# Optimization experiments

Measured on AMD Instinct MI355X. Metric: run time of the kernel, lower is better.

The kernel has to match this reference:

```python
import jax, jax.numpy as jnp
import numpy as np

L = 12; D = 768; H = 12; HD = 64; FF = 3072; P = 16; IMG = 224; BLK = 64
LORA = 16.0 / 64.0  # lora_alpha / r
PD = 512; B = 8


def _ln(x, g, b, eps=1e-6):
    m = x.mean(-1, keepdims=True)
    v = ((x - m) ** 2).mean(-1, keepdims=True)
    return (x - m) * jax.lax.rsqrt(v + eps) * g + b


def _dq(q, s):
    # int4 codes [O, I] + blockwise absmax-style scales [O, I//BLK] -> fp32 weight
    O, I = q.shape
    return ((q.astype(jnp.float32).reshape(O, I // BLK, BLK) - 7.5) * s[:, :, None]).reshape(O, I)


def _forward(img, patch_w, patch_b, cls_token, ln1_g, ln1_b, ln2_g, ln2_b, g1, g2,
             qkv_s, qkv_b, a_qkv, b_qkv, proj_s, proj_b, a_proj, b_proj,
             fc1_s, fc1_b, fc2_s, fc2_b, fcn_g, fcn_b, head_w, head_b,
             qkv_q, proj_q, fc1_q, fc2_q):
    x = img[:, 0]                                   # [B,3,224,224]
    Bn = x.shape[0]
    gp = IMG // P
    # patch embed (conv16x16/s16 == unfold + matmul)
    p = x.reshape(Bn, 3, gp, P, gp, P).transpose(0, 2, 4, 1, 3, 5).reshape(Bn, gp * gp, 3 * P * P)
    tok = p @ patch_w.T + patch_b                   # [B,196,768]
    cls = jnp.broadcast_to(cls_token, (Bn, 1, D))
    x = jnp.concatenate([cls, tok], axis=1)         # [B,197,768]

    def block(x, pr):
        (l1g, l1b, l2g, l2b, gm1, gm2, qq, qs, qb, aQ, bQ,
         pq, ps, pb, aP, bP, f1q, f1s, f1b, f2q, f2s, f2b) = pr
        h = _ln(x, l1g, l1b)
        # fused dequant + matmul + LoRA (qkv)
        qkv = h @ _dq(qq, qs).T + qb + LORA * ((h @ aQ.T) @ bQ.T)  # [B,N,3D]
        q, k, v = jnp.split(qkv, 3, axis=-1)
        heads = lambda t: t.reshape(Bn, -1, H, HD).transpose(0, 2, 1, 3)
        q, k, v = heads(q), heads(k), heads(v)
        attn = jax.nn.softmax(jnp.einsum('bhnd,bhmd->bhnm', q, k) / np.sqrt(HD).astype(np.float32), axis=-1)
        o = jnp.einsum('bhnm,bhmd->bhnd', attn, v).transpose(0, 2, 1, 3).reshape(Bn, -1, D)
        # dequant + matmul + LoRA (attn out proj)
        o = o @ _dq(pq, ps).T + pb + LORA * ((o @ aP.T) @ bP.T)
        x = x + gm1 * o                             # layerscale residual
        h = _ln(x, l2g, l2b)
        h = jax.nn.gelu(h @ _dq(f1q, f1s).T + f1b)
        h = h @ _dq(f2q, f2s).T + f2b
        x = x + gm2 * h
        return x, None

    xs = (ln1_g, ln1_b, ln2_g, ln2_b, g1, g2, qkv_q, qkv_s, qkv_b, a_qkv, b_qkv,
          proj_q, proj_s, proj_b, a_proj, b_proj, fc1_q, fc1_s, fc1_b, fc2_q, fc2_s, fc2_b)
    x, _ = jax.lax.scan(block, x, xs)
    pooled = x[:, 1:].mean(axis=1)                  # BEiT avg-pool over patch tokens
    pooled = _ln(pooled, fcn_g, fcn_b)              # fc_norm
    return jax.nn.relu(pooled @ head_w.T + head_b)  # Linear + ReLU projection -> [B,512]


def setup_inputs() -> dict:
    key = jax.random.key(0)
    ks = jax.random.split(key, 24)
    f = lambda i, sh, sc=0.02: jax.random.normal(ks[i], sh, dtype=jnp.float32) * sc
    u = lambda i, sh: jax.random.uniform(ks[i], sh, dtype=jnp.float32) * 0.01 + 1e-3
    qi = lambda i, sh: jax.random.randint(ks[i], sh, 0, 16, dtype=jnp.int32)
    return {
        'img': f(0, (B, 1, 3, IMG, IMG), 1.0),
        'patch_w': f(1, (D, 3 * P * P)), 'patch_b': jnp.zeros((D,), jnp.float32),
        'cls_token': f(2, (1, 1, D)),
        'ln1_g': jnp.ones((L, D), jnp.float32), 'ln1_b': jnp.zeros((L, D), jnp.float32),
        'ln2_g': jnp.ones((L, D), jnp.float32), 'ln2_b': jnp.zeros((L, D), jnp.float32),
        'g1': jnp.full((L, D), 0.1, jnp.float32), 'g2': jnp.full((L, D), 0.1, jnp.float32),
        'qkv_q': qi(3, (L, 3 * D, D)), 'qkv_s': u(4, (L, 3 * D, D // BLK)), 'qkv_b': f(5, (L, 3 * D)),
        'a_qkv': f(6, (L, 64, D)), 'b_qkv': f(7, (L, 3 * D, 64)),
        'proj_q': qi(8, (L, D, D)), 'proj_s': u(9, (L, D, D // BLK)), 'proj_b': jnp.zeros((L, D), jnp.float32),
        'a_proj': f(10, (L, 64, D)), 'b_proj': f(11, (L, D, 64)),
        'fc1_q': qi(12, (L, FF, D)), 'fc1_s': u(13, (L, FF, D // BLK)), 'fc1_b': jnp.zeros((L, FF), jnp.float32),
        'fc2_q': qi(14, (L, D, FF)), 'fc2_s': u(15, (L, D, FF // BLK)), 'fc2_b': jnp.zeros((L, D), jnp.float32),
        'fcn_g': jnp.ones((D,), jnp.float32), 'fcn_b': jnp.zeros((D,), jnp.float32),
        'head_w': f(16, (PD, D)), 'head_b': jnp.zeros((PD,), jnp.float32),
    }


def reference(img, patch_w, patch_b, cls_token, ln1_g, ln1_b, ln2_g, ln2_b, g1, g2,
              qkv_q, qkv_s, qkv_b, a_qkv, b_qkv, proj_q, proj_s, proj_b, a_proj, b_proj,
              fc1_q, fc1_s, fc1_b, fc2_q, fc2_s, fc2_b, fcn_g, fcn_b, head_w, head_b):
    return _forward(img, patch_w, patch_b, cls_token, ln1_g, ln1_b, ln2_g, ln2_b, g1, g2,
                    qkv_s, qkv_b, a_qkv, b_qkv, proj_s, proj_b, a_proj, b_proj,
                    fc1_s, fc1_b, fc2_s, fc2_b, fcn_g, fcn_b, head_w, head_b,
                    qkv_q, proj_q, fc1_q, fc2_q)
```

## Files before the change

### kernel.cpp

```cpp
#include <hip/hip_runtime.h>
#include <hip/hip_bf16.h>

using bf16 = __hip_bfloat16;
typedef __attribute__((ext_vector_type(8))) short short8;
typedef __attribute__((ext_vector_type(4))) float f32x4;

#define NTOK 197
#define MTOK 1576
#define MPATCH 1568
#define UROWS 102400

static __device__ __forceinline__ float bf2f(bf16 v){ return __bfloat162float(v); }
static __device__ __forceinline__ bf16 f2bf(float v){ return __float2bfloat16(v); }
static __device__ __forceinline__ unsigned pk2(float a, float b){
  union{ bf16 h[2]; unsigned u; } r; r.h[0]=f2bf(a); r.h[1]=f2bf(b); return r.u;
}

static __device__ __forceinline__ float gelu_tanh(float x){
  float x3 = x*x*x;
  float a = 0.7978845608028654f*(x + 0.044715f*x3);
  float e = __expf(-2.f*fabsf(a));
  float t = (1.f-e)/(1.f+e);
  t = (a >= 0.f) ? t : -t;
  return 0.5f*x*(1.f+t);
}

static __device__ __forceinline__ void gload16(const void* g, void* l){
  __builtin_amdgcn_global_load_lds(
      (const __attribute__((address_space(1))) unsigned*)g,
      (__attribute__((address_space(3))) unsigned*)l, 16, 0, 0);
}

template<int N> static __device__ __forceinline__ void wait_vm(){
  if constexpr (N==3)      asm volatile("s_waitcnt vmcnt(3)" ::: "memory");
  else if constexpr (N==5) asm volatile("s_waitcnt vmcnt(5)" ::: "memory");
  else                     asm volatile("s_waitcnt vmcnt(0)" ::: "memory");
}

__global__ void dq_k(const int* __restrict__ q, const float* __restrict__ s,
                     bf16* __restrict__ o, int rows, int K){
  long total8 = (long)rows * K / 8;
  for (long i = blockIdx.x*256 + threadIdx.x; i < total8; i += (long)gridDim.x*256){
    long e0 = i*8;
    int n = (int)(e0 / K), k = (int)(e0 % K);
    int4 a = *(const int4*)(q + (size_t)n*K + k);
    int4 b = *(const int4*)(q + (size_t)n*K + k + 4);
    float sc = s[(size_t)n*(K>>6) + (k>>6)];
    uint4 r;
    r.x = pk2(((float)a.x-7.5f)*sc, ((float)a.y-7.5f)*sc);
    r.y = pk2(((float)a.z-7.5f)*sc, ((float)a.w-7.5f)*sc);
    r.z = pk2(((float)b.x-7.5f)*sc, ((float)b.y-7.5f)*sc);
    r.w = pk2(((float)b.z-7.5f)*sc, ((float)b.w-7.5f)*sc);
    *(uint4*)(o + (size_t)n*K + k) = r;
  }
}

__global__ void cvt_k(const float* __restrict__ in, bf16* __restrict__ out, int n4){
  for (int i = blockIdx.x*256 + threadIdx.x; i < n4; i += gridDim.x*256){
    float4 v = *(const float4*)(in + (size_t)i*4);
    uint2 r; r.x = pk2(v.x, v.y); r.y = pk2(v.z, v.w);
    *(uint2*)(out + (size_t)i*4) = r;
  }
}

__global__ void usum_k(const float* __restrict__ part, bf16* __restrict__ ub){
  int i = blockIdx.x*256 + threadIdx.x;
  if (i >= MTOK*64/4) return;
  float4 s = {0.f,0.f,0.f,0.f};
  #pragma unroll
  for (int pz=0;pz<4;pz++){
    float4 v = *(const float4*)(part + (size_t)pz*UROWS + (size_t)i*4);
    s.x+=v.x; s.y+=v.y; s.z+=v.z; s.w+=v.w;
  }
  uint2 r; r.x = pk2(0.25f*s.x, 0.25f*s.y); r.y = pk2(0.25f*s.z, 0.25f*s.w);
  *(uint2*)(ub + (size_t)i*4) = r;
}

__global__ void patchify_k(const float* __restrict__ img, bf16* __restrict__ p){
  int idx = blockIdx.x*256 + threadIdx.x;
  if (idx >= MPATCH*768) return;
  int col = idx % 768, pr = idx / 768;
  int b = pr / 196, patch = pr % 196;
  int c = col >> 8, rem = col & 255, py = rem >> 4, px = rem & 15;
  int gy = patch / 14, gx = patch % 14;
  float v = img[(((size_t)(b*3 + c))*224 + gy*16 + py)*224 + gx*16 + px];
  p[idx] = f2bf(v);
}

__global__ void assemble_k(const float* __restrict__ tok, const float* __restrict__ cls,
                           float* __restrict__ x){
  int idx = blockIdx.x*256 + threadIdx.x;
  if (idx >= MTOK*768) return;
  int d = idx % 768, row = idx / 768;
  int b = row / NTOK, r = row % NTOK;
  x[idx] = (r == 0) ? cls[d] : tok[((size_t)(b*196) + r - 1)*768 + d];
}

__global__ __launch_bounds__(256) void ln_k(const float* __restrict__ x,
                                            const float* __restrict__ g,
                                            const float* __restrict__ b,
                                            bf16* __restrict__ out, int M){
  int row = blockIdx.x*4 + (threadIdx.x >> 6);
  int lane = threadIdx.x & 63;
  if (row >= M) return;
  const float* xr = x + (size_t)row*768;
  float4 v[3]; float s = 0.f;
  #pragma unroll
  for (int j=0;j<3;j++){
    v[j] = *(const float4*)(xr + lane*4 + j*256);
    s += v[j].x + v[j].y + v[j].z + v[j].w;
  }
  #pragma unroll
  for (int o=32;o;o>>=1) s += __shfl_xor(s, o);
  float mean = s * (1.f/768.f);
  float vs = 0.f;
  #pragma unroll
  for (int j=0;j<3;j++){
    float dx=v[j].x-mean, dy=v[j].y-mean, dz=v[j].z-mean, dw=v[j].w-mean;
    vs += dx*dx + dy*dy + dz*dz + dw*dw;
  }
  #pragma unroll
  for (int o=32;o;o>>=1) vs += __shfl_xor(vs, o);
  float rs = rsqrtf(vs*(1.f/768.f) + 1e-6f);
  bf16* orow = out + (size_t)row*768;
  #pragma unroll
  for (int j=0;j<3;j++){
    int d0 = lane*4 + j*256;
    float4 gv = *(const float4*)(g + d0);
    float4 bv = *(const float4*)(b + d0);
    uint2 pk;
    pk.x = pk2((v[j].x-mean)*rs*gv.x + bv.x, (v[j].y-mean)*rs*gv.y + bv.y);
    pk.y = pk2((v[j].z-mean)*rs*gv.z + bv.z, (v[j].w-mean)*rs*gv.w + bv.w);
    *(uint2*)(orow + d0) = pk;
  }
}

__global__ __launch_bounds__(256) void attn_k(const bf16* __restrict__ qkv, bf16* __restrict__ o){
  __shared__ char Kc[2][32*128];
  __shared__ bf16 Vt[2][64][40];
  __shared__ bf16 Pl[4][32][40];

  const int blk = blockIdx.x;
  const int half = blk & 1, bh = blk >> 1;
  const int b = bh / 12, h = bh % 12;
  const int t = threadIdx.x, wave = t>>6, lane = t&63;
  const int qbase = half*128 + wave*32;
  const bf16* base = qkv + (size_t)b*NTOK*2304 + h*64;

  short8 qf[2][2];
  #pragma unroll
  for (int qt=0;qt<2;qt++){
    int row = qbase + qt*16 + (lane&15); row = row < NTOK ? row : NTOK-1;
    const bf16* qr = base + (size_t)row*2304 + (lane>>4)*8;
    qf[qt][0] = *(const short8*)(qr);
    qf[qt][1] = *(const short8*)(qr + 32);
  }

  f32x4 Oa[2][4];
  float mrow[2][4], srow[2][4];
  #pragma unroll
  for (int i=0;i<2;i++)
    #pragma unroll
    for (int j=0;j<4;j++){ Oa[i][j] = (f32x4){0.f,0.f,0.f,0.f}; }
  #pragma unroll
  for (int i=0;i<2;i++)
    #pragma unroll
    for (int j=0;j<4;j++){ mrow[i][j] = -1e30f; srow[i][j] = 0.f; }

  const int sr = t>>3, sc = (t&7)*8;
  auto ldK = [&](int c)->uint4{
    int kv = c*32 + sr; kv = kv < NTOK ? kv : NTOK-1;
    return *(const uint4*)(base + (size_t)kv*2304 + 768 + sc);
  };
  auto ldV = [&](int c)->uint4{
    int kv = c*32 + sr;
    uint4 r = {0,0,0,0};
    if (kv < NTOK) r = *(const uint4*)(base + (size_t)kv*2304 + 1536 + sc);
    return r;
  };
  auto wrK = [&](int buf, uint4 kvv){
    *(uint4*)(Kc[buf] + sr*128 + ((sc*2) ^ ((sr&7)<<4))) = kvv;
  };
  auto wrV = [&](int buf, uint4 vvv){
    union{ uint4 u; short s[8]; } w; w.u = vvv;
    #pragma unroll
    for (int j=0;j<8;j++) *(short*)&Vt[buf][sc+j][sr] = w.s[j];
  };

  { uint4 k0 = ldK(0), v0 = ldV(0); wrK(0,k0); wrV(0,v0); }
  __syncthreads();

  for (int c=0;c<7;c++){
    const int buf = c & 1;
    uint4 kn, vn; const bool pf = (c < 6);
    if (pf){ kn = ldK(c+1); vn = ldV(c+1); }

    f32x4 S[2][2];
    #pragma unroll
    for (int i=0;i<2;i++)
      #pragma unroll
      for (int j=0;j<2;j++) S[i][j] = (f32x4){0.f,0.f,0.f,0.f};
    #pragma unroll
    for (int kt=0;kt<2;kt++){
      int rk = kt*16 + (lane&15);
      const char* kb = Kc[buf] + rk*128;
      int swz = (rk&7)<<4;
      short8 b0 = *(const short8*)(kb + (((lane>>4)*16) ^ swz));
      short8 b1 = *(const short8*)(kb + ((64 + (lane>>4)*16) ^ swz));
      #pragma unroll
      for (int qt=0;qt<2;qt++){
        S[qt][kt] = __builtin_amdgcn_mfma_f32_16x16x32_bf16(qf[qt][0], b0, S[qt][kt],0,0,0);
        S[qt][kt] = __builtin_amdgcn_mfma_f32_16x16x32_bf16(qf[qt][1], b1, S[qt][kt],0,0,0);
      }
    }

    #pragma unroll
    for (int qt=0;qt<2;qt++){
      #pragma unroll
      for (int r=0;r<4;r++){
        float s0 = S[qt][0][r]*0.125f, s1 = S[qt][1][r]*0.125f;
        if (c == 6){
          if (192 + (lane&15) >= NTOK) s0 = -1e30f;
          s1 = -1e30f;
        }
        float mx = fmaxf(s0, s1);
        mx = fmaxf(mx, __shfl_xor(mx,1));
        mx = fmaxf(mx, __shfl_xor(mx,2));
        mx = fmaxf(mx, __shfl_xor(mx,4));
        mx = fmaxf(mx, __shfl_xor(mx,8));
        float mo = mrow[qt][r];
        float mn = fmaxf(mo, mx);
        float scl = __expf(mo - mn);
        mrow[qt][r] = mn;
        float p0 = __expf(s0 - mn), p1 = __expf(s1 - mn);
        srow[qt][r] = srow[qt][r]*scl + p0 + p1;
        #pragma unroll
        for (int dt=0;dt<4;dt++) Oa[qt][dt][r] *= scl;
        int pr = qt*16 + (lane>>4)*4 + r;
        Pl[wave][pr][lane&15]      = f2bf(p0);
        Pl[wave][pr][16+(lane&15)] = f2bf(p1);
      }
    }

    short8 vb[4];
    #pragma unroll
    for (int dt=0;dt<4;dt++)
      vb[dt] = *(const short8*)(&Vt[buf][dt*16+(lane&15)][(lane>>4)*8]);
    #pragma unroll
    for (int qt=0;qt<2;qt++){
      short8 pa = *(const short8*)(&Pl[wave][qt*16+(lane&15)][(lane>>4)*8]);
      #pragma unroll
      for (int dt=0;dt<4;dt++)
        Oa[qt][dt] = __builtin_amdgcn_mfma_f32_16x16x32_bf16(pa, vb[dt], Oa[qt][dt],0,0,0);
    }

    if (pf){ wrK(buf^1, kn); wrV(buf^1, vn); }
    __syncthreads();
  }

  #pragma unroll
  for (int qt=0;qt<2;qt++)
    #pragma unroll
    for (int r=0;r<4;r++){
      float s = srow[qt][r];
      s += __shfl_xor(s,1); s += __shfl_xor(s,2);
      s += __shfl_xor(s,4); s += __shfl_xor(s,8);
      srow[qt][r] = 1.f/s;
    }
  #pragma unroll
  for (int qt=0;qt<2;qt++){
    #pragma unroll
    for (int r=0;r<4;r++){
      int tok = qbase + qt*16 + (lane>>4)*4 + r;
      if (tok < NTOK){
        bf16* orow = o + ((size_t)(b*NTOK+tok))*768 + h*64 + (lane&15);
        float inv = srow[qt][r];
        #pragma unroll
        for (int dt=0;dt<4;dt++) orow[dt*16] = f2bf(Oa[qt][dt][r]*inv);
      }
    }
  }
}

__global__ void pool_k(const float* __restrict__ x, float* __restrict__ pooled){
  int idx = blockIdx.x*256 + threadIdx.x;
  if (idx >= 8*768) return;
  int b = idx / 768, d = idx % 768;
  float s = 0.f;
  for (int i=1;i<NTOK;i++) s += x[((size_t)(b*NTOK)+i)*768 + d];
  pooled[idx] = s * (1.f/196.f);
}

template<int BM, int BN, int LORA, int OUTMODE, int ACT>
__global__ __launch_bounds__(256) void gemm_k(
    const bf16* __restrict__ A, const bf16* __restrict__ W,
    const bf16* __restrict__ ulora, const bf16* __restrict__ Blora,
    const float* __restrict__ bias, const float* __restrict__ gvec,
    void* __restrict__ Cout,
    int M, int N, int Kst, int kiters, size_t kslab)
{
  constexpr int WCM = BM/2;
  constexpr int WCN = BN/2;
  constexpr int FM  = WCM/16;
  constexpr int FN  = WCN/16;
  constexpr int NW  = BN/32;
  constexpr int LCNT = 1 + NW;

  __shared__ char As[2][BM*128];
  __shared__ char Bs[2][BN*128];

  int mt, nt;
  {
    int gmy = gridDim.y;
    int nwg = gridDim.x * gmy;
    int bid = blockIdx.y * gridDim.x + blockIdx.x;
    int q8 = nwg >> 3, r8 = nwg & 7, xcd = bid & 7, idx = bid >> 3;
    int swz = (xcd < r8 ? xcd*(q8+1) : r8*(q8+1) + (xcd-r8)*q8) + idx;
    nt = swz / gmy; mt = swz - nt*gmy;
  }
  const int kz = blockIdx.z;
  const int k0 = kz * kiters;
  const int t = threadIdx.x, wave = t>>6, lane = t&63;
  const int wr = wave>>1, wc = wave&1;
  const int KT = kiters + (LORA ? 1 : 0);

  const int srow = t >> 3;
  const int swzc = ((t&7)<<4) ^ ((srow&7)<<4);

  f32x4 acc[FM][FN];
  #pragma unroll
  for (int i=0;i<FM;i++)
    #pragma unroll
    for (int j=0;j<FN;j++) acc[i][j] = (f32x4){0.f,0.f,0.f,0.f};

  auto STAGE = [&](int it, int buf){
    {
      int gm = mt*BM + srow; gm = gm < M ? gm : M-1;
      const char* src = (LORA && it == kiters)
        ? (const char*)ulora + (size_t)gm*128 + swzc
        : (const char*)A + (size_t)gm*Kst*2 + (size_t)(k0+it)*128 + swzc;
      gload16(src, As[buf] + wave*1024);
    }
    #pragma unroll
    for (int c=0;c<NW;c++){
      int gn = nt*BN + 32*c + srow;
      const char* src = (LORA && it == kiters)
        ? (const char*)Blora + (size_t)gn*128 + swzc
        : (const char*)W + (size_t)gn*Kst*2 + (size_t)(k0+it)*128 + swzc;
      gload16(src, Bs[buf] + c*4096 + wave*1024);
    }
  };

  const int lrow = lane & 15;
  const int lkb  = (lane >> 4) * 16;
  auto computeTile = [&](int buf){
    __builtin_amdgcn_s_setprio(1);
    #pragma unroll
    for (int kk=0; kk<2; kk++){
      short8 af[FM]; short8 bw[FN];
      #pragma unroll
      for (int f=0; f<FM; f++){
        int ra = wr*WCM + f*16 + lrow;
        af[f] = *(const short8*)(As[buf] + ra*128 + ((kk*64 + lkb) ^ ((ra&7)<<4)));
      }
      #pragma unroll
      for (int f=0; f<FN; f++){
        int rb = wc*WCN + f*16 + lrow;
        bw[f] = *(const short8*)(Bs[buf] + rb*128 + ((kk*64 + lkb) ^ ((rb&7)<<4)));
      }
      #pragma unroll
      for (int i=0;i<FM;i++)
        #pragma unroll
        for (int j=0;j<FN;j++)
          acc[i][j] = __builtin_amdgcn_mfma_f32_16x16x32_bf16(af[i], bw[j], acc[i][j], 0, 0, 0);
    }
    __builtin_amdgcn_s_setprio(0);
  };

  STAGE(0, 0);
  if (KT > 1) STAGE(1, 1);

  for (int it = 0; it < KT; ++it){
    if (it == KT-1) wait_vm<0>(); else wait_vm<LCNT>();
    __builtin_amdgcn_s_barrier();
    computeTile(it & 1);
    asm volatile("s_waitcnt lgkmcnt(0)" ::: "memory");
    __builtin_amdgcn_s_barrier();
    if (it+2 < KT) STAGE(it+2, it & 1);
  }

  const int erow = (lane >> 4) * 4, ecol = lane & 15;
  #pragma unroll
  for (int i=0;i<FM;i++){
    #pragma unroll
    for (int j=0;j<FN;j++){
      int n = nt*BN + wc*WCN + j*16 + ecol;
      float bv = (bias != nullptr) ? bias[n] : 0.f;
      float gv = (OUTMODE==2) ? gvec[n] : 0.f;
      #pragma unroll
      for (int q=0; q<4; q++){
        int m = mt*BM + wr*WCM + i*16 + erow + q;
        if (m < M){
          float v = acc[i][j][q] + bv;
          if (ACT == 1) v = gelu_tanh(v);
          if (ACT == 2) v = fmaxf(v, 0.f);
          size_t off = (size_t)m*N + n;
          if (OUTMODE == 0)      ((float*)Cout)[(size_t)kz*kslab + off] = v;
          else if (OUTMODE == 1) ((bf16*)Cout)[off] = f2bf(v);
          else                   ((float*)Cout)[off] += gv * v;
        }
      }
    }
  }
}

extern "C" void kernel_launch(void* const* d_in, const int* in_sizes, int n_in,
                              void* d_out, int out_size, void* d_ws, size_t ws_size,
                              hipStream_t stream){
  (void)in_sizes; (void)n_in; (void)out_size; (void)ws_size;
  const float* img    = (const float*)d_in[0];
  const float* patchw = (const float*)d_in[1];
  const float* patchb = (const float*)d_in[2];
  const float* cls    = (const float*)d_in[3];
  const float* ln1g   = (const float*)d_in[4];
  const float* ln1b   = (const float*)d_in[5];
  const float* ln2g   = (const float*)d_in[6];
  const float* ln2b   = (const float*)d_in[7];
  const float* g1     = (const float*)d_in[8];
  const float* g2     = (const float*)d_in[9];
  const int*   qkvq   = (const int*)d_in[10];
  const float* qkvs   = (const float*)d_in[11];
  const float* qkvb   = (const float*)d_in[12];
  const float* aQ     = (const float*)d_in[13];
  const float* bQ     = (const float*)d_in[14];
  const int*   projq  = (const int*)d_in[15];
  const float* projs  = (const float*)d_in[16];
  const float* projb  = (const float*)d_in[17];
  const float* aP     = (const float*)d_in[18];
  const float* bP     = (const float*)d_in[19];
  const int*   fc1q   = (const int*)d_in[20];
  const float* fc1s   = (const float*)d_in[21];
  const float* fc1b   = (const float*)d_in[22];
  const int*   fc2q   = (const int*)d_in[23];
  const float* fc2s   = (const float*)d_in[24];
  const float* fc2b   = (const float*)d_in[25];
  const float* fcn_g  = (const float*)d_in[26];
  const float* fcn_b  = (const float*)d_in[27];
  const float* headw  = (const float*)d_in[28];
  const float* headb  = (const float*)d_in[29];
  float* out = (float*)d_out;

  char* wp = (char*)d_ws;
  auto alloc = [&](size_t bytes)->char* {
    char* r = wp; wp += (bytes + 255) & ~(size_t)255; return r;
  };
  float* x      = (float*)alloc((size_t)MTOK*768*4);
  bf16*  qkvo   = (bf16*) alloc((size_t)MTOK*2304*2);
  bf16*  h      = (bf16*) alloc((size_t)MTOK*768*2);
  bf16*  h1     = (bf16*) alloc((size_t)MTOK*3072*2);
  bf16*  ob     = (bf16*) alloc((size_t)MTOK*768*2);
  float* u_part = (float*)alloc((size_t)4*UROWS*4);
  bf16*  ub     = (bf16*) alloc((size_t)MTOK*64*2);
  bf16*  p      = (bf16*) alloc((size_t)MPATCH*768*2);
  float* tmp    = (float*)alloc((size_t)MTOK*768*4);
  float* pooled = (float*)alloc((size_t)8*768*4);
  bf16*  pooledb= (bf16*) alloc((size_t)8*768*2);
  bf16* wqb = (bf16*)alloc((size_t)12*2304*768*2);
  bf16* wpb = (bf16*)alloc((size_t)12*768*768*2);
  bf16* w1b = (bf16*)alloc((size_t)12*3072*768*2);
  bf16* w2b = (bf16*)alloc((size_t)12*768*3072*2);
  bf16* patchwb = (bf16*)alloc((size_t)768*768*2);
  bf16* headwb  = (bf16*)alloc((size_t)512*768*2);
  bf16* aQb = (bf16*)alloc((size_t)12*64*768*2);
  bf16* bQb = (bf16*)alloc((size_t)12*2304*64*2);
  bf16* aPb = (bf16*)alloc((size_t)12*64*768*2);
  bf16* bPb = (bf16*)alloc((size_t)12*768*64*2);

  const int GM32 = (MTOK + 31) / 32;

  dq_k<<<2048, 256, 0, stream>>>(qkvq, qkvs, wqb, 12*2304, 768);
  dq_k<<<2048, 256, 0, stream>>>(projq, projs, wpb, 12*768, 768);
  dq_k<<<2048, 256, 0, stream>>>(fc1q, fc1s, w1b, 12*3072, 768);
  dq_k<<<2048, 256, 0, stream>>>(fc2q, fc2s, w2b, 12*768, 3072);
  cvt_k<<<576, 256, 0, stream>>>(patchw, patchwb, 768*768/4);
  cvt_k<<<384, 256, 0, stream>>>(headw, headwb, 512*768/4);
  cvt_k<<<576, 256, 0, stream>>>(aQ, aQb, 12*64*768/4);
  cvt_k<<<1728, 256, 0, stream>>>(bQ, bQb, 12*2304*64/4);
  cvt_k<<<576, 256, 0, stream>>>(aP, aPb, 12*64*768/4);
  cvt_k<<<576, 256, 0, stream>>>(bP, bPb, 12*768*64/4);

  patchify_k<<<(MPATCH*768 + 255)/256, 256, 0, stream>>>(img, p);
  gemm_k<32,64,0,0,0><<<dim3(768/64, MPATCH/32, 1), 256, 0, stream>>>(
      p, patchwb, nullptr, nullptr, patchb, nullptr, tmp,
      MPATCH, 768, 768, 12, 0);
  assemble_k<<<(MTOK*768 + 255)/256, 256, 0, stream>>>(tmp, cls, x);

  for (int l=0; l<12; l++){
    const bf16* wq_l = wqb + (size_t)l*2304*768;
    const bf16* wp_l = wpb + (size_t)l*768*768;
    const bf16* w1_l = w1b + (size_t)l*3072*768;
    const bf16* w2_l = w2b + (size_t)l*768*3072;

    ln_k<<<(MTOK+3)/4, 256, 0, stream>>>(x, ln1g + l*768, ln1b + l*768, h, MTOK);
    gemm_k<32,64,0,0,0><<<dim3(1, GM32, 4), 256, 0, stream>>>(
        h, aQb + (size_t)l*64*768, nullptr, nullptr, nullptr, nullptr, u_part,
        MTOK, 64, 768, 3, UROWS);
    usum_k<<<(MTOK*64/4 + 255)/256, 256, 0, stream>>>(u_part, ub);
    gemm_k<32,128,1,1,0><<<dim3(2304/128, GM32, 1), 256, 0, stream>>>(
        h, wq_l, ub, bQb + (size_t)l*2304*64, qkvb + (size_t)l*2304,
        nullptr, qkvo, MTOK, 2304, 768, 12, 0);
    attn_k<<<192, 256, 0, stream>>>(qkvo, ob);
    gemm_k<32,64,0,0,0><<<dim3(1, GM32, 4), 256, 0, stream>>>(
        ob, aPb + (size_t)l*64*768, nullptr, nullptr, nullptr, nullptr, u_part,
        MTOK, 64, 768, 3, UROWS);
    usum_k<<<(MTOK*64/4 + 255)/256, 256, 0, stream>>>(u_part, ub);
    gemm_k<32,64,1,2,0><<<dim3(768/64, GM32, 1), 256, 0, stream>>>(
        ob, wp_l, ub, bPb + (size_t)l*768*64, projb + (size_t)l*768,
        g1 + l*768, x, MTOK, 768, 768, 12, 0);

    ln_k<<<(MTOK+3)/4, 256, 0, stream>>>(x, ln2g + l*768, ln2b + l*768, h, MTOK);
    gemm_k<32,128,0,1,1><<<dim3(3072/128, GM32, 1), 256, 0, stream>>>(
        h, w1_l, nullptr, nullptr, fc1b + (size_t)l*3072,
        nullptr, h1, MTOK, 3072, 768, 12, 0);
    gemm_k<32,64,0,2,0><<<dim3(768/64, GM32, 1), 256, 0, stream>>>(
        h1, w2_l, nullptr, nullptr, fc2b + (size_t)l*768,
        g2 + l*768, x, MTOK, 768, 3072, 48, 0);
  }

  pool_k<<<(8*768 + 255)/256, 256, 0, stream>>>(x, pooled);
  ln_k<<<2, 256, 0, stream>>>(pooled, fcn_g, fcn_b, pooledb, 8);
  gemm_k<32,128,0,0,2><<<dim3(512/128, 1, 1), 256, 0, stream>>>(
      pooledb, headwb, nullptr, nullptr, headb, nullptr, out,
      8, 512, 768, 12, 0);
}
```

Baseline: 1.739 ms.

## Fold LoRA adapters into dequantized qkv and proj weights once at setup

Computes W + 0.25*B@A for the qkv and output-projection weights with a per-layer batched GEMM during setup, and adds the result into the bf16 dequantized weights. The per-layer LoRA down-projection GEMMs, partial-sum reductions and the extra LoRA k-step in the main GEMMs are removed. The cost is one extra setup GEMM over all layers and an additional bf16 rounding of the merged weight, which may shift numerics slightly.

```diff
diff --git a/kernel.cpp b/kernel.cpp
--- a/kernel.cpp
+++ b/kernel.cpp
@@ -8,7 +8,6 @@
 #define NTOK 197
 #define MTOK 1576
 #define MPATCH 1568
-#define UROWS 102400
 
 static __device__ __forceinline__ float bf2f(bf16 v){ return __bfloat162float(v); }
 static __device__ __forceinline__ bf16 f2bf(float v){ return __float2bfloat16(v); }
@@ -55,25 +54,23 @@
   }
 }
 
-__global__ void cvt_k(const float* __restrict__ in, bf16* __restrict__ out, int n4){
+__global__ void cvt_k(const float* __restrict__ in, bf16* __restrict__ out, int n4, float a){
   for (int i = blockIdx.x*256 + threadIdx.x; i < n4; i += gridDim.x*256){
     float4 v = *(const float4*)(in + (size_t)i*4);
-    uint2 r; r.x = pk2(v.x, v.y); r.y = pk2(v.z, v.w);
+    uint2 r; r.x = pk2(v.x*a, v.y*a); r.y = pk2(v.z*a, v.w*a);
     *(uint2*)(out + (size_t)i*4) = r;
   }
 }
 
-__global__ void usum_k(const float* __restrict__ part, bf16* __restrict__ ub){
-  int i = blockIdx.x*256 + threadIdx.x;
-  if (i >= MTOK*64/4) return;
-  float4 s = {0.f,0.f,0.f,0.f};
-  #pragma unroll
-  for (int pz=0;pz<4;pz++){
-    float4 v = *(const float4*)(part + (size_t)pz*UROWS + (size_t)i*4);
-    s.x+=v.x; s.y+=v.y; s.z+=v.z; s.w+=v.w;
-  }
-  uint2 r; r.x = pk2(0.25f*s.x, 0.25f*s.y); r.y = pk2(0.25f*s.z, 0.25f*s.w);
-  *(uint2*)(ub + (size_t)i*4) = r;
+__global__ void trans_k(const float* __restrict__ in, bf16* __restrict__ out,
+                        int L, int R, int C){
+  long total = (long)L*R*C;
+  for (long i = blockIdx.x*256 + threadIdx.x; i < total; i += (long)gridDim.x*256){
+    long rc = (long)R*C;
+    int l = (int)(i / rc); long rem = i % rc;
+    int c = (int)(rem / R), r = (int)(rem % R);
+    out[i] = f2bf(in[(size_t)l*rc + (size_t)r*C + c]);
+  }
 }
 
 __global__ void patchify_k(const float* __restrict__ img, bf16* __restrict__ p){
@@ -291,10 +288,9 @@
   pooled[idx] = s * (1.f/196.f);
 }
 
-template<int BM, int BN, int LORA, int OUTMODE, int ACT>
+template<int BM, int BN, int OUTMODE, int ACT, int FOLD>
 __global__ __launch_bounds__(256) void gemm_k(
     const bf16* __restrict__ A, const bf16* __restrict__ W,
-    const bf16* __restrict__ ulora, const bf16* __restrict__ Blora,
     const float* __restrict__ bias, const float* __restrict__ gvec,
     void* __restrict__ Cout,
     int M, int N, int Kst, int kiters, size_t kslab)
@@ -318,11 +314,15 @@
     int swz = (xcd < r8 ? xcd*(q8+1) : r8*(q8+1) + (xcd-r8)*q8) + idx;
     nt = swz / gmy; mt = swz - nt*gmy;
   }
-  const int kz = blockIdx.z;
+  if (FOLD){
+    A += (size_t)blockIdx.z * (size_t)M * 64;
+    W += (size_t)blockIdx.z * (size_t)N * 64;
+  }
+  const int kz = FOLD ? 0 : blockIdx.z;
   const int k0 = kz * kiters;
   const int t = threadIdx.x, wave = t>>6, lane = t&63;
   const int wr = wave>>1, wc = wave&1;
-  const int KT = kiters + (LORA ? 1 : 0);
+  const int KT = kiters;
 
   const int srow = t >> 3;
   const int swzc = ((t&7)<<4) ^ ((srow&7)<<4);
@@ -336,18 +336,14 @@
   auto STAGE = [&](int it, int buf){
     {
       int gm = mt*BM + srow; gm = gm < M ? gm : M-1;
-      const char* src = (LORA && it == kiters)
-        ? (const char*)ulora + (size_t)gm*128 + swzc
-        : (const char*)A + (size_t)gm*Kst*2 + (size_t)(k0+it)*128 + swzc;
-      gload16(src, As[buf] + wave*1024);
+      gload16((const char*)A + (size_t)gm*Kst*2 + (size_t)(k0+it)*128 + swzc,
+              As[buf] + wave*1024);
     }
     #pragma unroll
     for (int c=0;c<NW;c++){
       int gn = nt*BN + 32*c + srow;
-      const char* src = (LORA && it == kiters)
-        ? (const char*)Blora + (size_t)gn*128 + swzc
-        : (const char*)W + (size_t)gn*Kst*2 + (size_t)(k0+it)*128 + swzc;
-      gload16(src, Bs[buf] + c*4096 + wave*1024);
+      gload16((const char*)W + (size_t)gn*Kst*2 + (size_t)(k0+it)*128 + swzc,
+              Bs[buf] + c*4096 + wave*1024);
     }
   };
 
@@ -407,7 +403,11 @@
           size_t off = (size_t)m*N + n;
           if (OUTMODE == 0)      ((float*)Cout)[(size_t)kz*kslab + off] = v;
           else if (OUTMODE == 1) ((bf16*)Cout)[off] = f2bf(v);
-          else                   ((float*)Cout)[off] += gv * v;
+          else if (OUTMODE == 2) ((float*)Cout)[off] += gv * v;
+          else {
+            bf16* C = (bf16*)Cout + (FOLD ? (size_t)blockIdx.z*(size_t)M*N : (size_t)0);
+            C[off] = f2bf(bf2f(C[off]) + v);
+          }
         }
       }
     }
@@ -459,8 +459,6 @@
   bf16*  h      = (bf16*) alloc((size_t)MTOK*768*2);
   bf16*  h1     = (bf16*) alloc((size_t)MTOK*3072*2);
   bf16*  ob     = (bf16*) alloc((size_t)MTOK*768*2);
-  float* u_part = (float*)alloc((size_t)4*UROWS*4);
-  bf16*  ub     = (bf16*) alloc((size_t)MTOK*64*2);
   bf16*  p      = (bf16*) alloc((size_t)MPATCH*768*2);
   float* tmp    = (float*)alloc((size_t)MTOK*768*4);
   float* pooled = (float*)alloc((size_t)8*768*4);
@@ -471,10 +469,10 @@
   bf16* w2b = (bf16*)alloc((size_t)12*768*3072*2);
   bf16* patchwb = (bf16*)alloc((size_t)768*768*2);
   bf16* headwb  = (bf16*)alloc((size_t)512*768*2);
-  bf16* aQb = (bf16*)alloc((size_t)12*64*768*2);
-  bf16* bQb = (bf16*)alloc((size_t)12*2304*64*2);
-  bf16* aPb = (bf16*)alloc((size_t)12*64*768*2);
-  bf16* bPb = (bf16*)alloc((size_t)12*768*64*2);
+  bf16* bQs = (bf16*)alloc((size_t)12*2304*64*2);
+  bf16* bPs = (bf16*)alloc((size_t)12*768*64*2);
+  bf16* aQT = (bf16*)alloc((size_t)12*768*64*2);
+  bf16* aPT = (bf16*)alloc((size_t)12*768*64*2);
 
   const int GM32 = (MTOK + 31) / 32;
 
@@ -482,17 +480,20 @@
   dq_k<<<2048, 256, 0, stream>>>(projq, projs, wpb, 12*768, 768);
   dq_k<<<2048, 256, 0, stream>>>(fc1q, fc1s, w1b, 12*3072, 768);
   dq_k<<<2048, 256, 0, stream>>>(fc2q, fc2s, w2b, 12*768, 3072);
-  cvt_k<<<576, 256, 0, stream>>>(patchw, patchwb, 768*768/4);
-  cvt_k<<<384, 256, 0, stream>>>(headw, headwb, 512*768/4);
-  cvt_k<<<576, 256, 0, stream>>>(aQ, aQb, 12*64*768/4);
-  cvt_k<<<1728, 256, 0, stream>>>(bQ, bQb, 12*2304*64/4);
-  cvt_k<<<576, 256, 0, stream>>>(aP, aPb, 12*64*768/4);
-  cvt_k<<<576, 256, 0, stream>>>(bP, bPb, 12*768*64/4);
+  cvt_k<<<576, 256, 0, stream>>>(patchw, patchwb, 768*768/4, 1.f);
+  cvt_k<<<384, 256, 0, stream>>>(headw, headwb, 512*768/4, 1.f);
+  cvt_k<<<1728, 256, 0, stream>>>(bQ, bQs, 12*2304*64/4, 0.25f);
+  cvt_k<<<576, 256, 0, stream>>>(bP, bPs, 12*768*64/4, 0.25f);
+  trans_k<<<1024, 256, 0, stream>>>(aQ, aQT, 12, 64, 768);
+  trans_k<<<1024, 256, 0, stream>>>(aP, aPT, 12, 64, 768);
+  gemm_k<32,64,3,0,1><<<dim3(768/64, 2304/32, 12), 256, 0, stream>>>(
+      bQs, aQT, nullptr, nullptr, wqb, 2304, 768, 64, 1, 0);
+  gemm_k<32,64,3,0,1><<<dim3(768/64, 768/32, 12), 256, 0, stream>>>(
+      bPs, aPT, nullptr, nullptr, wpb, 768, 768, 64, 1, 0);
 
   patchify_k<<<(MPATCH*768 + 255)/256, 256, 0, stream>>>(img, p);
   gemm_k<32,64,0,0,0><<<dim3(768/64, MPATCH/32, 1), 256, 0, stream>>>(
-      p, patchwb, nullptr, nullptr, patchb, nullptr, tmp,
-      MPATCH, 768, 768, 12, 0);
+      p, patchwb, patchb, nullptr, tmp, MPATCH, 768, 768, 12, 0);
   assemble_k<<<(MTOK*768 + 255)/256, 256, 0, stream>>>(tmp, cls, x);
 
   for (int l=0; l<12; l++){
@@ -502,34 +503,21 @@
     const bf16* w2_l = w2b + (size_t)l*768*3072;
 
     ln_k<<<(MTOK+3)/4, 256, 0, stream>>>(x, ln1g + l*768, ln1b + l*768, h, MTOK);
-    gemm_k<32,64,0,0,0><<<dim3(1, GM32, 4), 256, 0, stream>>>(
-        h, aQb + (size_t)l*64*768, nullptr, nullptr, nullptr, nullptr, u_part,
-        MTOK, 64, 768, 3, UROWS);
-    usum_k<<<(MTOK*64/4 + 255)/256, 256, 0, stream>>>(u_part, ub);
-    gemm_k<32,128,1,1,0><<<dim3(2304/128, GM32, 1), 256, 0, stream>>>(
-        h, wq_l, ub, bQb + (size_t)l*2304*64, qkvb + (size_t)l*2304,
-        nullptr, qkvo, MTOK, 2304, 768, 12, 0);
+    gemm_k<32,128,1,0,0><<<dim3(2304/128, GM32, 1), 256, 0, stream>>>(
+        h, wq_l, qkvb + (size_t)l*2304, nullptr, qkvo, MTOK, 2304, 768, 12, 0);
     attn_k<<<192, 256, 0, stream>>>(qkvo, ob);
-    gemm_k<32,64,0,0,0><<<dim3(1, GM32, 4), 256, 0, stream>>>(
-        ob, aPb + (size_t)l*64*768, nullptr, nullptr, nullptr, nullptr, u_part,
-        MTOK, 64, 768, 3, UROWS);
-    usum_k<<<(MTOK*64/4 + 255)/256, 256, 0, stream>>>(u_part, ub);
-    gemm_k<32,64,1,2,0><<<dim3(768/64, GM32, 1), 256, 0, stream>>>(
-        ob, wp_l, ub, bPb + (size_t)l*768*64, projb + (size_t)l*768,
-        g1 + l*768, x, MTOK, 768, 768, 12, 0);
+    gemm_k<32,64,2,0,0><<<dim3(768/64, GM32, 1), 256, 0, stream>>>(
+        ob, wp_l, projb + (size_t)l*768, g1 + l*768, x, MTOK, 768, 768, 12, 0);
 
     ln_k<<<(MTOK+3)/4, 256, 0, stream>>>(x, ln2g + l*768, ln2b + l*768, h, MTOK);
-    gemm_k<32,128,0,1,1><<<dim3(3072/128, GM32, 1), 256, 0, stream>>>(
-        h, w1_l, nullptr, nullptr, fc1b + (size_t)l*3072,
-        nullptr, h1, MTOK, 3072, 768, 12, 0);
-    gemm_k<32,64,0,2,0><<<dim3(768/64, GM32, 1), 256, 0, stream>>>(
-        h1, w2_l, nullptr, nullptr, fc2b + (size_t)l*768,
-        g2 + l*768, x, MTOK, 768, 3072, 48, 0);
+    gemm_k<32,128,1,1,0><<<dim3(3072/128, GM32, 1), 256, 0, stream>>>(
+        h, w1_l, fc1b + (size_t)l*3072, nullptr, h1, MTOK, 3072, 768, 12, 0);
+    gemm_k<32,64,2,0,0><<<dim3(768/64, GM32, 1), 256, 0, stream>>>(
+        h1, w2_l, fc2b + (size_t)l*768, g2 + l*768, x, MTOK, 768, 3072, 48, 0);
   }
 
   pool_k<<<(8*768 + 255)/256, 256, 0, stream>>>(x, pooled);
   ln_k<<<2, 256, 0, stream>>>(pooled, fcn_g, fcn_b, pooledb, 8);
-  gemm_k<32,128,0,0,2><<<dim3(512/128, 1, 1), 256, 0, stream>>>(
-      pooledb, headwb, nullptr, nullptr, headb, nullptr, out,
-      8, 512, 768, 12, 0);
-}
+  gemm_k<32,128,0,2,0><<<dim3(512/128, 1, 1), 256, 0, stream>>>(
+      pooledb, headwb, headb, nullptr, out, 8, 512, 768, 12, 0);
+}
```

After: 1.595 ms. 8.2% less time.
